# Performance work log

Hardware: AMD Instinct MI355X
Metric: run time of the kernel (lower is better)

The kernel has to match this reference:

```python
import jax, jax.numpy as jnp
import numpy as np

B, S, D, UNITS = 4, 2048, 4096, 4096

def setup_inputs() -> dict:
    key = jax.random.key(0)
    k1, k2 = jax.random.split(key)
    x = jax.random.normal(k1, (B, S, D), dtype=jnp.float32)
    # int8 quantized kernel, values in [-127, 127]
    quantized_kernel = jax.random.randint(k2, (D, UNITS), -127, 128, dtype=jnp.int32).astype(jnp.int8)
    scale = jnp.float32(0.02)
    return {"x": x, "quantized_kernel": quantized_kernel, "scale": scale}

def reference(x, quantized_kernel, scale):
    # Dequantize int8 weights to fp32 and apply linear transform: y = x @ (W_int8 * scale)
    kernel_fp32 = quantized_kernel.astype(jnp.float32) * scale
    return jnp.einsum("bsd,du->bsu", x, kernel_fp32)
```

## Files before the change

### kernel.cpp

```cpp
#include <hip/hip_runtime.h>
#include <cstdint>

typedef unsigned short u16;
typedef __bf16 bf16x8 __attribute__((ext_vector_type(8)));
typedef float f32x4 __attribute__((ext_vector_type(4)));
typedef int   i32x4 __attribute__((ext_vector_type(4)));
typedef u16   u16x4 __attribute__((ext_vector_type(4)));

#define M_DIM 8192
#define N_DIM 4096
#define K_DIM 4096

#define GLOBAL_AS(p) ((const __attribute__((address_space(1))) void*)(p))
#define LDS_AS(p)    ((__attribute__((address_space(3))) void*)(p))

__device__ __forceinline__ u16 f2bf(float f) {
    union { float f; uint32_t u; } x; x.f = f;
    uint32_t u = x.u;
    uint32_t r = (u + 0x7fffu + ((u >> 16) & 1u)) >> 16;
    return (u16)r;
}

__global__ __launch_bounds__(256) void prepass_kernel(const float* __restrict__ X,
                                                      const int* __restrict__ W,
                                                      u16* __restrict__ Xb,
                                                      u16* __restrict__ Wt) {
    const int bid = blockIdx.x;
    const int t   = threadIdx.x;
    if (bid < 4096) {
        __shared__ int tile[64][65];
        const int n0 = (bid & 63) * 64;
        const int k0 = (bid >> 6) * 64;
#pragma unroll
        for (int i = 0; i < 4; i++) {
            int e = t + i * 256;
            int r = e >> 4;
            int c = (e & 15) * 4;
            i32x4 v = __builtin_nontemporal_load(
                (const i32x4*)(W + (size_t)(k0 + r) * N_DIM + n0 + c));
            tile[r][c] = v.x; tile[r][c + 1] = v.y; tile[r][c + 2] = v.z; tile[r][c + 3] = v.w;
        }
        __syncthreads();
        {
            int n = t >> 2, ks = (t & 3) * 16;
            __align__(16) u16 o[16];
#pragma unroll
            for (int i = 0; i < 16; i++)
                o[i] = f2bf((float)tile[ks + i][n]);
            u16* dst = Wt + (size_t)(n0 + n) * K_DIM + k0 + ks;
            *(uint4*)(dst)     = *(const uint4*)&o[0];
            *(uint4*)(dst + 8) = *(const uint4*)&o[8];
        }
    } else {
        const size_t base = (size_t)(bid - 4096) * 4096;
        const f32x4*   x4 = (const f32x4*)X;
        u16x4*         o4 = (u16x4*)Xb;
#pragma unroll
        for (int it = 0; it < 8; it++) {
            size_t ia = base + (size_t)it * 512 + t;
            size_t ib = ia + 256;
            f32x4 a = __builtin_nontemporal_load(x4 + ia);
            f32x4 b = __builtin_nontemporal_load(x4 + ib);
            u16x4 oa, ob;
            oa.x = f2bf(a.x); oa.y = f2bf(a.y); oa.z = f2bf(a.z); oa.w = f2bf(a.w);
            ob.x = f2bf(b.x); ob.y = f2bf(b.y); ob.z = f2bf(b.z); ob.w = f2bf(b.w);
            o4[ia] = oa;
            o4[ib] = ob;
        }
    }
}


#define BK 64
#define NT (K_DIM / BK)
static_assert(NT >= 6 && (NT & 1) == 0, "tile count must be even and >= 6");

#define BARRIER() do { asm volatile("" ::: "memory"); \
                       __builtin_amdgcn_s_barrier();  \
                       asm volatile("" ::: "memory"); } while (0)
#define WAIT_LGKM() asm volatile("s_waitcnt lgkmcnt(0)" ::: "memory")
#define VMCNT(n)    asm volatile("s_waitcnt vmcnt(" #n ")" ::: "memory")

#define READ_A(dst, base, mhv)                                                    \
    _Pragma("unroll") for (int i = 0; i < 4; i++) {                               \
        const char* p_ = (base) + ((mhv) * 128 + wrow * 64 + i * 16 + fr) * 128;  \
        _Pragma("unroll") for (int kk = 0; kk < 2; kk++)                          \
            dst[i][kk] = *(const bf16x8*)(p_ + ((kk * 64 + fk2) ^ sw));           \
    }

#define READ_B(dst, base, nhv)                                                    \
    _Pragma("unroll") for (int j = 0; j < 2; j++) {                               \
        const char* p_ = (base) + ((nhv) * 128 + wcol * 32 + j * 16 + fr) * 128;  \
        _Pragma("unroll") for (int kk = 0; kk < 2; kk++)                          \
            dst[j][kk] = *(const bf16x8*)(p_ + ((kk * 64 + fk2) ^ sw));           \
    }

#define MFMA_Q(MH, NH, aarr, barr)                                                \
    do {                                                                          \
        __builtin_amdgcn_s_setprio(1);                                            \
        _Pragma("unroll") for (int kk = 0; kk < 2; kk++)                          \
            _Pragma("unroll") for (int i = 0; i < 4; i++)                         \
                _Pragma("unroll") for (int j = 0; j < 2; j++)                     \
                    acc[MH][NH][i][j] = __builtin_amdgcn_mfma_f32_16x16x32_bf16(  \
                        aarr[i][kk], barr[j][kk], acc[MH][NH][i][j], 0, 0, 0);    \
        __builtin_amdgcn_s_setprio(0);                                            \
    } while (0)

#define STAGE_A(bufv, h, kt)                                                      \
    do {                                                                          \
        const u16* g_ = gA + (size_t)(h) * (128 * K_DIM) + (size_t)(kt) * 64;     \
        char* l_ = (char*)lds + (bufv) * 32768 + (h) * 16384 + wv * 1024;         \
        __builtin_amdgcn_global_load_lds(GLOBAL_AS(g_ + aoff0), LDS_AS(l_), 16, 0, 0);        \
        __builtin_amdgcn_global_load_lds(GLOBAL_AS(g_ + aoff1), LDS_AS(l_ + 8192), 16, 0, 0); \
    } while (0)

#define STAGE_B(bufv, h, kt)                                                      \
    do {                                                                          \
        const u16* g_ = gB + (size_t)(h) * (128 * K_DIM) + (size_t)(kt) * 64;     \
        char* l_ = (char*)lds + 65536 + (bufv) * 32768 + (h) * 16384 + wv * 1024; \
        __builtin_amdgcn_global_load_lds(GLOBAL_AS(g_ + aoff0), LDS_AS(l_), 16, 0, 0);        \
        __builtin_amdgcn_global_load_lds(GLOBAL_AS(g_ + aoff1), LDS_AS(l_ + 8192), 16, 0, 0); \
    } while (0)

#define TILE(bv, S1, S2, S3, S4, VM2, PRE)                                        \
    {                                                                             \
        const char* As_ = (const char*)lds + (bv) * 32768;                        \
        const char* Bs_ = (const char*)lds + 65536 + (bv) * 32768;                \
        const char* An_ = (const char*)lds + ((bv) ^ 1) * 32768;                  \
        const char* Bn_ = (const char*)lds + 65536 + ((bv) ^ 1) * 32768;          \
                                                                         \
        BARRIER(); WAIT_LGKM();                                                   \
        READ_B(b1, Bs_, 1);                                                       \
        S1;                                                                       \
        MFMA_Q(0, 0, a0, b0);                                                     \
                                                                         \
        BARRIER(); WAIT_LGKM();                                                   \
        READ_A(a1, As_, 1);                                                       \
        S2; VM2;                                                                  \
        MFMA_Q(0, 1, a0, b1);                                                     \
                                                                         \
        BARRIER(); WAIT_LGKM();                                                   \
        if (PRE) { READ_A(a0, An_, 0); }                                          \
        S3;                                                                       \
        MFMA_Q(1, 0, a1, b0);                                                     \
                                                                         \
        BARRIER(); WAIT_LGKM();                                                   \
        if (PRE) { READ_B(b0, Bn_, 0); }                                          \
        S4;                                                                       \
        MFMA_Q(1, 1, a1, b1);                                                     \
    }

__global__ __launch_bounds__(512, 2) void gemm_bf16_kernel(const u16* __restrict__ A,
                                                           const u16* __restrict__ Bt,
                                                           const float* __restrict__ scale_p,
                                                           float* __restrict__ C) {
    __shared__ __align__(16) u16 lds[65536];

    const int tid  = threadIdx.x;
    const int lane = tid & 63;
    const int wv   = tid >> 6;
    const int wrow = wv >> 2;
    const int wcol = wv & 3;

    const int bid = blockIdx.x;
    const int wg  = ((bid & 7) << 6) | (bid >> 3);
    const size_t m0 = (size_t)(wg >> 4) * 256;
    const size_t n0 = (size_t)(wg & 15) * 256;

    const int fr  = lane & 15;
    const int fk2 = (lane >> 4) * 16;
    const int sw  = (lane & 7) << 4;

    const int q0 = tid,       r0 = q0 >> 3, c0 = (q0 & 7) ^ (r0 & 7);
    const int q1 = tid + 512, r1 = q1 >> 3, c1 = (q1 & 7) ^ (r1 & 7);
    const size_t aoff0 = (size_t)r0 * K_DIM + c0 * 8;
    const size_t aoff1 = (size_t)r1 * K_DIM + c1 * 8;

    const u16* gA = A  + m0 * K_DIM;
    const u16* gB = Bt + n0 * K_DIM;

    f32x4 acc[2][2][4][2] = {};
    bf16x8 a0[4][2], a1[4][2], b0[2][2], b1[2][2];

    STAGE_A(0, 0, 0); STAGE_B(0, 0, 0); STAGE_B(0, 1, 0); STAGE_A(0, 1, 0);
    STAGE_A(1, 0, 1); STAGE_B(1, 0, 1); STAGE_B(1, 1, 1); STAGE_A(1, 1, 1);
    VMCNT(8);
    BARRIER();
    {
        const char* As_ = (const char*)lds;
        const char* Bs_ = (const char*)lds + 65536;
        READ_A(a0, As_, 0);
        READ_B(b0, Bs_, 0);
    }
    WAIT_LGKM();

    for (int T = 0; T < NT - 2; T += 2) {
        TILE(0,
             STAGE_A(0, 0, T + 2), STAGE_B(0, 0, T + 2),
             STAGE_B(0, 1, T + 2), STAGE_A(0, 1, T + 2),
             VMCNT(4), 1);
        TILE(1,
             STAGE_A(1, 0, T + 3), STAGE_B(1, 0, T + 3),
             STAGE_B(1, 1, T + 3), STAGE_A(1, 1, T + 3),
             VMCNT(4), 1);
    }
    TILE(0, (void)0, (void)0, (void)0, (void)0, VMCNT(0), 1);
    TILE(1, (void)0, (void)0, (void)0, (void)0, (void)0, 0);

    const float s = *scale_p;
    const int ec = lane & 15;
    const int er = (lane >> 4) * 4;
#pragma unroll
    for (int mh = 0; mh < 2; mh++)
#pragma unroll
        for (int nh = 0; nh < 2; nh++)
#pragma unroll
            for (int i = 0; i < 4; i++)
#pragma unroll
                for (int j = 0; j < 2; j++) {
                    float* cp = C + (m0 + mh * 128 + wrow * 64 + i * 16 + er) * N_DIM
                                  + (n0 + nh * 128 + wcol * 32 + j * 16 + ec);
#pragma unroll
                    for (int r = 0; r < 4; r++)
                        __builtin_nontemporal_store(acc[mh][nh][i][j][r] * s,
                                                    cp + (size_t)r * N_DIM);
                }
}

__global__ __launch_bounds__(256) void fb_gemm_kernel(const float* __restrict__ X,
                                                      const int* __restrict__ W,
                                                      const float* __restrict__ sp,
                                                      float* __restrict__ Y) {
    __shared__ float Xs[16][64];
    __shared__ float Ws[16][64];
    const int t = threadIdx.x;
    const int tx = t & 15, ty = t >> 4;
    const int m0 = blockIdx.y * 64, n0 = blockIdx.x * 64;
    float acc[4][4] = {};
    for (int k0 = 0; k0 < K_DIM; k0 += 16) {
#pragma unroll
        for (int i = 0; i < 4; i++) {
            int e = t + i * 256;
            int r = e >> 4, c = e & 15;
            Xs[c][r] = X[(size_t)(m0 + r) * K_DIM + k0 + c];
            int rw = e >> 6, cw = e & 63;
            Ws[rw][cw] = (float)W[(size_t)(k0 + rw) * N_DIM + n0 + cw];
        }
        __syncthreads();
#pragma unroll
        for (int kk = 0; kk < 16; kk++)
#pragma unroll
            for (int i = 0; i < 4; i++)
#pragma unroll
                for (int j = 0; j < 4; j++)
                    acc[i][j] += Xs[kk][ty * 4 + i] * Ws[kk][tx * 4 + j];
        __syncthreads();
    }
    const float s = *sp;
#pragma unroll
    for (int i = 0; i < 4; i++)
#pragma unroll
        for (int j = 0; j < 4; j++)
            Y[(size_t)(m0 + ty * 4 + i) * N_DIM + n0 + tx * 4 + j] = acc[i][j] * s;
}

extern "C" void kernel_launch(void* const* d_in, const int* in_sizes, int n_in,
                              void* d_out, int out_size, void* d_ws, size_t ws_size,
                              hipStream_t stream) {
    const float* X  = (const float*)d_in[0];
    const int*   W  = (const int*)d_in[1];
    const float* sp = (const float*)d_in[2];
    float* Y = (float*)d_out;

    const size_t xb = (size_t)M_DIM * K_DIM * sizeof(u16);
    const size_t wb = (size_t)N_DIM * K_DIM * sizeof(u16);

    if (ws_size >= xb + wb) {
        u16* Xb = (u16*)d_ws;
        u16* Wt = (u16*)((char*)d_ws + xb);
        prepass_kernel<<<6144, 256, 0, stream>>>(X, W, Xb, Wt);
        gemm_bf16_kernel<<<512, 512, 0, stream>>>(Xb, Wt, sp, Y);
    } else {
        fb_gemm_kernel<<<dim3(N_DIM / 64, M_DIM / 64), 256, 0, stream>>>(X, W, sp, Y);
    }
}
```

Measured before the change: 515.9 us.

## Reschedule GEMM main loop with split A-fragment reads and delayed A staging

Splits the A-fragment LDS reads into low and high halves and interleaves them with the MFMA quadrants, so each quadrant's operands are fetched just before use. It delays staging of the second A half-tile by one tile and relaxes the vmcnt wait from 4 to 6 to deepen overlap between global-to-LDS copies and compute. The cost is roughly twice as many workgroup barriers per tile. The aim is lower register pressure and less memory-wait stall. The prologue still stages that half-tile, so it is loaded twice on the first iteration.

```diff
diff --git a/kernel.cpp b/kernel.cpp
--- a/kernel.cpp
+++ b/kernel.cpp
@@ -81,13 +81,18 @@
 #define WAIT_LGKM() asm volatile("s_waitcnt lgkmcnt(0)" ::: "memory")
 #define VMCNT(n)    asm volatile("s_waitcnt vmcnt(" #n ")" ::: "memory")
 
-#define READ_A(dst, base, mhv)                                                    \
-    _Pragma("unroll") for (int i = 0; i < 4; i++) {                               \
+#define READ_A_LO(dst, base, mhv)                                                 \
+    _Pragma("unroll") for (int i = 0; i < 2; i++) {                               \
         const char* p_ = (base) + ((mhv) * 128 + wrow * 64 + i * 16 + fr) * 128;  \
         _Pragma("unroll") for (int kk = 0; kk < 2; kk++)                          \
             dst[i][kk] = *(const bf16x8*)(p_ + ((kk * 64 + fk2) ^ sw));           \
     }
-
+#define READ_A_HI(dst, base, mhv)                                                 \
+    _Pragma("unroll") for (int i = 2; i < 4; i++) {                               \
+        const char* p_ = (base) + ((mhv) * 128 + wrow * 64 + i * 16 + fr) * 128;  \
+        _Pragma("unroll") for (int kk = 0; kk < 2; kk++)                          \
+            dst[i][kk] = *(const bf16x8*)(p_ + ((kk * 64 + fk2) ^ sw));           \
+    }
 #define READ_B(dst, base, nhv)                                                    \
     _Pragma("unroll") for (int j = 0; j < 2; j++) {                               \
         const char* p_ = (base) + ((nhv) * 128 + wcol * 32 + j * 16 + fr) * 128;  \
@@ -122,32 +127,38 @@
         __builtin_amdgcn_global_load_lds(GLOBAL_AS(g_ + aoff1), LDS_AS(l_ + 8192), 16, 0, 0); \
     } while (0)
 
-#define TILE(bv, S1, S2, S3, S4, VM2, PRE)                                        \
+#define TILE(bv, S1, S2, S3, S4, SYNC, PRE)                                       \
     {                                                                             \
         const char* As_ = (const char*)lds + (bv) * 32768;                        \
         const char* Bs_ = (const char*)lds + 65536 + (bv) * 32768;                \
         const char* An_ = (const char*)lds + ((bv) ^ 1) * 32768;                  \
         const char* Bn_ = (const char*)lds + 65536 + ((bv) ^ 1) * 32768;          \
                                                                          \
+        READ_A_HI(a0, As_, 0);                                                    \
+        S1;                                                                       \
         BARRIER(); WAIT_LGKM();                                                   \
+        MFMA_Q(0, 0, a0, b0);                                                     \
+        BARRIER();                                                                \
+                                                                         \
         READ_B(b1, Bs_, 1);                                                       \
-        S1;                                                                       \
-        MFMA_Q(0, 0, a0, b0);                                                     \
-                                                                         \
+        READ_A_LO(a1, As_, 1);                                                    \
+        S2;                                                                       \
         BARRIER(); WAIT_LGKM();                                                   \
-        READ_A(a1, As_, 1);                                                       \
-        S2; VM2;                                                                  \
         MFMA_Q(0, 1, a0, b1);                                                     \
-                                                                         \
+        BARRIER();                                                                \
+                                                                         \
+        READ_A_HI(a1, As_, 1);                                                    \
+        S3;                                                                       \
         BARRIER(); WAIT_LGKM();                                                   \
-        if (PRE) { READ_A(a0, An_, 0); }                                          \
-        S3;                                                                       \
         MFMA_Q(1, 0, a1, b0);                                                     \
-                                                                         \
-        BARRIER(); WAIT_LGKM();                                                   \
-        if (PRE) { READ_B(b0, Bn_, 0); }                                          \
+        BARRIER();                                                                \
+                                                                         \
         S4;                                                                       \
+        BARRIER();                                                                \
         MFMA_Q(1, 1, a1, b1);                                                     \
+        SYNC;                                                                     \
+        if (PRE) { READ_B(b0, Bn_, 0); READ_A_LO(a0, An_, 0); }                   \
+        BARRIER();                                                                \
     }
 
 __global__ __launch_bounds__(512, 2) void gemm_bf16_kernel(const u16* __restrict__ A,
@@ -189,22 +200,22 @@
     {
         const char* As_ = (const char*)lds;
         const char* Bs_ = (const char*)lds + 65536;
-        READ_A(a0, As_, 0);
         READ_B(b0, Bs_, 0);
+        READ_A_LO(a0, As_, 0);
     }
     WAIT_LGKM();
 
     for (int T = 0; T < NT - 2; T += 2) {
         TILE(0,
-             STAGE_A(0, 0, T + 2), STAGE_B(0, 0, T + 2),
-             STAGE_B(0, 1, T + 2), STAGE_A(0, 1, T + 2),
-             VMCNT(4), 1);
+             STAGE_A(1, 1, T + 1), STAGE_A(0, 0, T + 2),
+             STAGE_B(0, 0, T + 2), STAGE_B(0, 1, T + 2),
+             VMCNT(6), 1);
         TILE(1,
-             STAGE_A(1, 0, T + 3), STAGE_B(1, 0, T + 3),
-             STAGE_B(1, 1, T + 3), STAGE_A(1, 1, T + 3),
-             VMCNT(4), 1);
-    }
-    TILE(0, (void)0, (void)0, (void)0, (void)0, VMCNT(0), 1);
+             STAGE_A(0, 1, T + 2), STAGE_A(1, 0, T + 3),
+             STAGE_B(1, 0, T + 3), STAGE_B(1, 1, T + 3),
+             VMCNT(6), 1);
+    }
+    TILE(0, STAGE_A(1, 1, NT - 1), (void)0, (void)0, (void)0, VMCNT(0), 1);
     TILE(1, (void)0, (void)0, (void)0, (void)0, (void)0, 0);
 
     const float s = *scale_p;
```

Result: faster. 466.6 us (-9.6%).
